# Kernel tuning notes

Measured on AMD Instinct MI355X. Metric: run time of the kernel, lower is better.

The kernel has to match this reference:

```python
import jax, jax.numpy as jnp
import numpy as np

DIM = 1024
HEADS = 16
DIM_HEAD = 64
SEQ = 2048
BATCH = 2
SCALE = DIM_HEAD ** -0.5
NEG = -jnp.finfo(jnp.float32).max


def setup_inputs() -> dict:
    key = jax.random.key(0)
    k1, k2, k3 = jax.random.split(key, 3)
    x = jax.random.normal(k1, (BATCH, SEQ, DIM), dtype=jnp.float32)
    w_qkv = jax.random.normal(k2, (DIM, 3 * HEADS * DIM_HEAD), dtype=jnp.float32) * 0.02
    w_out = jax.random.normal(k3, (HEADS * DIM_HEAD, DIM), dtype=jnp.float32) * 0.02
    b_out = jnp.zeros((DIM,), dtype=jnp.float32)
    return {"x": x, "w_qkv": w_qkv, "w_out": w_out, "b_out": b_out}


def reference(x, w_qkv, w_out, b_out):
    b, n, _ = x.shape
    qkv = x @ w_qkv  # [b, n, 3*h*d]
    q, k, v = jnp.split(qkv, 3, axis=-1)
    def to_heads(t):
        return t.reshape(b, n, HEADS, DIM_HEAD).transpose(0, 2, 1, 3)  # b h n d
    q, k, v = to_heads(q), to_heads(k), to_heads(v)
    q = q * SCALE
    dots = jnp.einsum('bhid,bhjd->bhij', q, k)  # materialized [b,h,n,n] scores
    causal_mask = jnp.triu(jnp.ones((n, n), dtype=bool), k=1)
    dots = jnp.where(causal_mask, NEG, dots)
    attn = jax.nn.softmax(dots, axis=-1)
    out = jnp.einsum('bhij,bhjd->bhid', attn, v)
    out = out.transpose(0, 2, 1, 3).reshape(b, n, HEADS * DIM_HEAD)
    return out @ w_out + b_out
```

## Files before the change

### kernel.cpp

```cpp
#include <hip/hip_runtime.h>
#include <cstdint>

typedef __attribute__((ext_vector_type(8))) short bfrag_t;
typedef __attribute__((ext_vector_type(4))) float f32x4_t;

#define MFMA16(a,b,c) __builtin_amdgcn_mfma_f32_16x16x32_bf16((a),(b),(c),0,0,0)

__device__ __forceinline__ unsigned short f2bf(float f){
  unsigned u = __float_as_uint(f);
  unsigned r = u + 0x7fffu + ((u >> 16) & 1u);
  return (unsigned short)(r >> 16);
}

__device__ __forceinline__ unsigned pk2bf(float a, float b){
  unsigned r;
  asm("v_cvt_pk_bf16_f32 %0, %1, %2" : "=v"(r) : "v"(a), "v"(b));
  return r;
}

__device__ __forceinline__ void gload16(const unsigned short* g, unsigned short* l){
  __builtin_amdgcn_global_load_lds(
      (const __attribute__((address_space(1))) unsigned int*)(const void*)g,
      (__attribute__((address_space(3))) unsigned int*)(void*)l,
      16, 0, 0);
}

__global__ __launch_bounds__(256) void k_cvt(const float* __restrict__ in,
                                             unsigned short* __restrict__ out, int n4){
  int i = blockIdx.x*blockDim.x + threadIdx.x;
  int stride = gridDim.x*blockDim.x;
  for(; i < n4; i += stride){
    float4 v = ((const float4*)in)[i];
    ushort4 o;
    o.x = f2bf(v.x); o.y = f2bf(v.y); o.z = f2bf(v.z); o.w = f2bf(v.w);
    ((ushort4*)out)[i] = o;
  }
}

__global__ __launch_bounds__(256) void k_transpose(const float* __restrict__ in,
                                                   unsigned short* __restrict__ out,
                                                   int R, int C){
  __shared__ unsigned short tile[32][33];
  int bc = blockIdx.x*32, br = blockIdx.y*32;
  int tx = threadIdx.x & 31, ty = threadIdx.x >> 5;
  #pragma unroll
  for(int i=0;i<32;i+=8){
    tile[ty+i][tx] = f2bf(in[(size_t)(br+ty+i)*C + bc + tx]);
  }
  __syncthreads();
  #pragma unroll
  for(int i=0;i<32;i+=8){
    out[(size_t)(bc+ty+i)*R + br + tx] = tile[tx][ty+i];
  }
}

__global__ __launch_bounds__(256) void k_gemm1(
    const unsigned short* __restrict__ A,
    const unsigned short* __restrict__ Bt,
    unsigned short* __restrict__ Qo, unsigned short* __restrict__ Kimg,
    unsigned short* __restrict__ Vimg)
{
  __shared__ unsigned short ldsA[128*64];
  __shared__ unsigned short ldsB[128*64];

  const int tid = threadIdx.x;
  const int lane = tid & 63;
  const int w = tid >> 6;
  const int wr = w >> 1, wc = w & 1;
  const int col16 = lane & 15, g = lane >> 4;
  const int bm = blockIdx.y * 128;
  const int bn = blockIdx.x * 128;
  const int K = 1024;
  const int SWAP = (bn < 2048) ? 1 : 0;

  f32x4_t acc[4][4];
  #pragma unroll
  for(int i=0;i<4;i++)
    #pragma unroll
    for(int j=0;j<4;j++) acc[i][j] = (f32x4_t)0.0f;

  for(int k0=0; k0<K; k0+=64){
    __syncthreads();
    #pragma unroll
    for(int i=0; i<4; i++){
      int u = i*256 + tid;
      int row = u>>3, s = u&7, gs = s ^ (row&7);
      gload16(A + (size_t)(bm+row)*K + k0 + gs*8, ldsA + (i*256 + w*64)*8);
    }
    #pragma unroll
    for(int i=0; i<4; i++){
      int u = i*256 + tid;
      int row = u>>3, s = u&7, gs = s ^ (row&7);
      gload16(Bt + (size_t)(bn+row)*K + k0 + gs*8, ldsB + (i*256 + w*64)*8);
    }
    __syncthreads();
    #pragma unroll
    for(int kk=0; kk<2; kk++){
      bfrag_t af[4], bfr[4];
      #pragma unroll
      for(int mi=0;mi<4;mi++){
        int row = wr*64 + mi*16 + col16;
        int slot = (kk*4 + g) ^ (row&7);
        af[mi] = *(const bfrag_t*)(ldsA + row*64 + slot*8);
      }
      #pragma unroll
      for(int ni=0;ni<4;ni++){
        int row = wc*64 + ni*16 + col16;
        int slot = (kk*4 + g) ^ (row&7);
        bfr[ni] = *(const bfrag_t*)(ldsB + row*64 + slot*8);
      }
      if (SWAP){
        #pragma unroll
        for(int mi=0;mi<4;mi++)
          #pragma unroll
          for(int ni=0;ni<4;ni++)
            acc[mi][ni] = MFMA16(bfr[ni], af[mi], acc[mi][ni]);
      } else {
        #pragma unroll
        for(int mi=0;mi<4;mi++)
          #pragma unroll
          for(int ni=0;ni<4;ni++)
            acc[mi][ni] = MFMA16(af[mi], bfr[ni], acc[mi][ni]);
      }
    }
  }

  if (bn < 2048){
    const int which = bn >> 10;
    #pragma unroll
    for(int mi=0;mi<4;mi++){
      int s_full = bm + wr*64 + mi*16 + col16;
      int b = s_full >> 11, sq = s_full & 2047;
      #pragma unroll
      for(int ni=0;ni<4;ni++){
        int n0 = bn + wc*64 + ni*16 + g*4;
        int h = (n0 & 1023) >> 6;
        int d0 = n0 & 63;
        size_t bh = (size_t)(b*16 + h);
        float v0 = acc[mi][ni][0], v1 = acc[mi][ni][1];
        float v2 = acc[mi][ni][2], v3 = acc[mi][ni][3];
        if (which == 0){
          const float sc = 0.18033688f;
          uint2 pkd; pkd.x = pk2bf(v0*sc, v1*sc); pkd.y = pk2bf(v2*sc, v3*sc);
          *(uint2*)(Qo + (bh*2048 + sq)*64 + d0) = pkd;
        } else {
          int kt = sq >> 6, rr = sq & 63;
          int ks = rr >> 4, c16i = rr & 15;
          int dk = d0 >> 5, g3 = (d0 >> 3) & 3, e0 = d0 & 7;
          uint2 pkd; pkd.x = pk2bf(v0, v1); pkd.y = pk2bf(v2, v3);
          size_t off = bh*131072 + (size_t)kt*4096
                     + (size_t)(ks*2 + dk)*512 + (size_t)(g3*16 + c16i)*8 + e0;
          *(uint2*)(Kimg + off) = pkd;
        }
      }
    }
  } else {
    #pragma unroll
    for(int mi=0;mi<4;mi++){
      int s0 = bm + wr*64 + mi*16 + g*4;
      int b = s0 >> 11, sq0 = s0 & 2047;
      int kt = sq0 >> 6, sc0 = sq0 & 63;
      int jk = sc0 >> 5, g3 = (sc0 >> 3) & 3, e0 = sc0 & 7;
      #pragma unroll
      for(int ni=0;ni<4;ni++){
        int ncol = bn + wc*64 + ni*16 + col16;
        int h = (ncol & 1023) >> 6;
        int d64 = ncol & 63;
        int nimg = d64 >> 4, c16i = d64 & 15;
        size_t bh = (size_t)(b*16 + h);
        uint2 pkd;
        pkd.x = pk2bf(acc[mi][ni][0], acc[mi][ni][1]);
        pkd.y = pk2bf(acc[mi][ni][2], acc[mi][ni][3]);
        size_t off = bh*131072 + (size_t)kt*4096
                   + (size_t)(nimg*2 + jk)*512 + (size_t)(g3*16 + c16i)*8 + e0;
        *(uint2*)(Vimg + off) = pkd;
      }
    }
  }
}

__global__ __launch_bounds__(256) void k_gemm2(
    const unsigned short* __restrict__ A,
    const unsigned short* __restrict__ Bt,
    float* __restrict__ Co, const float* __restrict__ bias)
{
  __shared__ unsigned short ldsA[64*64];
  __shared__ unsigned short ldsB[128*64];

  const int tid = threadIdx.x;
  const int lane = tid & 63;
  const int w = tid >> 6;
  const int wc = w;
  const int col16 = lane & 15, g = lane >> 4;
  const int bm = blockIdx.y * 64;
  const int bn = blockIdx.x * 128;
  const int K = 1024, N = 1024;

  f32x4_t acc[4][2];
  #pragma unroll
  for(int i=0;i<4;i++)
    #pragma unroll
    for(int j=0;j<2;j++) acc[i][j] = (f32x4_t)0.0f;

  for(int k0=0; k0<K; k0+=64){
    __syncthreads();
    #pragma unroll
    for(int i=0; i<2; i++){
      int u = i*256 + tid;
      int row = u>>3, s = u&7, gs = s ^ (row&7);
      gload16(A + (size_t)(bm+row)*K + k0 + gs*8, ldsA + (i*256 + w*64)*8);
    }
    #pragma unroll
    for(int i=0; i<4; i++){
      int u = i*256 + tid;
      int row = u>>3, s = u&7, gs = s ^ (row&7);
      gload16(Bt + (size_t)(bn+row)*K + k0 + gs*8, ldsB + (i*256 + w*64)*8);
    }
    __syncthreads();
    #pragma unroll
    for(int kk=0; kk<2; kk++){
      bfrag_t af[4], bfr[2];
      #pragma unroll
      for(int mi=0;mi<4;mi++){
        int row = mi*16 + col16;
        int slot = (kk*4 + g) ^ (row&7);
        af[mi] = *(const bfrag_t*)(ldsA + row*64 + slot*8);
      }
      #pragma unroll
      for(int ni=0;ni<2;ni++){
        int row = wc*32 + ni*16 + col16;
        int slot = (kk*4 + g) ^ (row&7);
        bfr[ni] = *(const bfrag_t*)(ldsB + row*64 + slot*8);
      }
      #pragma unroll
      for(int mi=0;mi<4;mi++)
        #pragma unroll
        for(int ni=0;ni<2;ni++)
          acc[mi][ni] = MFMA16(af[mi], bfr[ni], acc[mi][ni]);
    }
  }

  #pragma unroll
  for(int mi=0;mi<4;mi++){
    int mrow = bm + mi*16 + g*4;
    #pragma unroll
    for(int ni=0;ni<2;ni++){
      int ncol = bn + wc*32 + ni*16 + col16;
      float bb = bias[ncol];
      #pragma unroll
      for(int r=0;r<4;r++){
        Co[(size_t)(mrow+r)*N + ncol] = acc[mi][ni][r] + bb;
      }
    }
  }
}

__global__ __launch_bounds__(256, 4) void k_attn(
    const unsigned short* __restrict__ Q,
    const unsigned short* __restrict__ Kimg,
    const unsigned short* __restrict__ Vimg,
    unsigned short* __restrict__ O)
{
  __shared__ unsigned short kls[2*4096];
  __shared__ unsigned short vls[2*4096];
  __shared__ unsigned short plds[4*1024];
  const int lane = threadIdx.x & 63;
  const int w = threadIdx.x >> 6;
  const int col16 = lane & 15, g = lane >> 4;
  const int bh = blockIdx.x;
  const int y = blockIdx.y;
  const int idx = (y & 7)*4 + (y >> 3);
  const int qt = (idx & 1) ? (31 - (idx >> 1)) : (idx >> 1);
  const int b = bh >> 4, h = bh & 15;

  const unsigned short* Qb = Q    + (size_t)bh*2048*64;
  const unsigned short* Kb = Kimg + (size_t)bh*131072;
  const unsigned short* Vb = Vimg + (size_t)bh*131072;
  char* pw = (char*)(plds + w*1024);

  auto stage = [&](int kt, int bsel){
    const unsigned short* gk = Kb + (size_t)kt*4096;
    const unsigned short* gv = Vb + (size_t)kt*4096;
    unsigned short* lk = kls + bsel*4096;
    unsigned short* lv = vls + bsel*4096;
    #pragma unroll
    for(int c=0;c<2;c++){
      int chunk = w*2 + c;
      int u = chunk*64 + lane;
      gload16(gk + u*8, lk + chunk*512);
      gload16(gv + u*8, lv + chunk*512);
    }
  };

  const int qrow0 = qt*64 + w*16;
  const int nkt = qt + 1;
  const int qi = qrow0 + col16;

  bfrag_t qf[2];
  #pragma unroll
  for(int dk=0;dk<2;dk++)
    qf[dk] = *(const bfrag_t*)(Qb + (size_t)(qrow0 + col16)*64 + dk*32 + g*8);

  f32x4_t oaccT[4];
  #pragma unroll
  for(int n=0;n<4;n++) oaccT[n] = (f32x4_t)0.0f;
  float mrun = -1e30f, lrun = 0.f;

  stage(0, 0);
  __syncthreads();

  #pragma unroll 1
  for(int kt=0; kt<nkt; kt++){
    const int cur = kt & 1;
    if (kt+1 < nkt) stage(kt+1, cur^1);

    const bfrag_t* kb = (const bfrag_t*)(kls + cur*4096);
    const bfrag_t* vb = (const bfrag_t*)(vls + cur*4096);

    f32x4_t sacc[4];
    __builtin_amdgcn_s_setprio(1);
    #pragma unroll
    for(int ks=0; ks<4; ks++){
      bfrag_t kf0 = kb[(ks*2+0)*64 + lane];
      bfrag_t kf1 = kb[(ks*2+1)*64 + lane];
      f32x4_t c = (f32x4_t)0.0f;
      c = MFMA16(kf0, qf[0], c);
      c = MFMA16(kf1, qf[1], c);
      sacc[ks] = c;
    }
    __builtin_amdgcn_s_setprio(0);
    if (kt == qt){
      const int kbase = kt*64;
      #pragma unroll
      for(int ks=0; ks<4; ks++)
        #pragma unroll
        for(int r=0;r<4;r++){
          int kj = kbase + ks*16 + g*4 + r;
          if (kj > qi) sacc[ks][r] = -1e30f;
        }
    }
    float pm = fmaxf(
        fmaxf(fmaxf(fmaxf(sacc[0][0],sacc[0][1]),fmaxf(sacc[0][2],sacc[0][3])),
              fmaxf(fmaxf(sacc[1][0],sacc[1][1]),fmaxf(sacc[1][2],sacc[1][3]))),
        fmaxf(fmaxf(fmaxf(sacc[2][0],sacc[2][1]),fmaxf(sacc[2][2],sacc[2][3])),
              fmaxf(fmaxf(sacc[3][0],sacc[3][1]),fmaxf(sacc[3][2],sacc[3][3]))));
    pm = fmaxf(pm, __shfl_xor(pm, 16));
    pm = fmaxf(pm, __shfl_xor(pm, 32));
    if (!__all(pm - mrun <= 11.5415603f)){
      float mnew = fmaxf(mrun, pm);
      float alpha = __builtin_amdgcn_exp2f(mrun - mnew);
      mrun = mnew;
      lrun *= alpha;
      #pragma unroll
      for(int n=0;n<4;n++)
        #pragma unroll
        for(int r=0;r<4;r++)
          oaccT[n][r] *= alpha;
    }
    float rs = 0.f;
    #pragma unroll
    for(int ks=0; ks<4; ks++){
      float p0 = __builtin_amdgcn_exp2f(sacc[ks][0] - mrun);
      float p1 = __builtin_amdgcn_exp2f(sacc[ks][1] - mrun);
      float p2 = __builtin_amdgcn_exp2f(sacc[ks][2] - mrun);
      float p3 = __builtin_amdgcn_exp2f(sacc[ks][3] - mrun);
      rs += (p0+p1)+(p2+p3);
      unsigned w0 = pk2bf(p0, p1);
      unsigned w1 = pk2bf(p2, p3);
      int byte0 = (col16*128 + (ks*16 + g*4)*2) ^ ((col16&7)<<4);
      unsigned long long wd = ((unsigned long long)w1 << 32) | w0;
      *(unsigned long long*)(pw + byte0) = wd;
    }
    rs += __shfl_xor(rs, 16);
    rs += __shfl_xor(rs, 32);
    lrun += rs;
    bfrag_t pf[2];
    #pragma unroll
    for(int jk=0;jk<2;jk++){
      int byteo = (col16*128 + jk*64 + g*16) ^ ((col16&7)<<4);
      pf[jk] = *(const bfrag_t*)(pw + byteo);
    }
    __builtin_amdgcn_s_setprio(1);
    #pragma unroll
    for(int n=0;n<4;n++){
      bfrag_t v0 = vb[(n*2+0)*64 + lane];
      bfrag_t v1 = vb[(n*2+1)*64 + lane];
      oaccT[n] = MFMA16(v0, pf[0], oaccT[n]);
      oaccT[n] = MFMA16(v1, pf[1], oaccT[n]);
    }
    __builtin_amdgcn_s_setprio(0);
    __syncthreads();
  }

  {
    float inv = 1.0f / lrun;
    size_t obase = ((size_t)(b*2048 + qi))*1024 + (size_t)h*64;
    #pragma unroll
    for(int n=0;n<4;n++){
      uint2 pkd;
      pkd.x = pk2bf(oaccT[n][0]*inv, oaccT[n][1]*inv);
      pkd.y = pk2bf(oaccT[n][2]*inv, oaccT[n][3]*inv);
      *(uint2*)(O + obase + n*16 + g*4) = pkd;
    }
  }
}

extern "C" void kernel_launch(void* const* d_in, const int* in_sizes, int n_in,
                              void* d_out, int out_size, void* d_ws, size_t ws_size,
                              hipStream_t stream){
  const float* x     = (const float*)d_in[0];
  const float* w_qkv = (const float*)d_in[1];
  const float* w_out = (const float*)d_in[2];
  const float* b_out = (const float*)d_in[3];
  float* out = (float*)d_out;

  unsigned char* ws = (unsigned char*)d_ws;
  unsigned short* xbf   = (unsigned short*)(ws);
  unsigned short* wqkvT = (unsigned short*)(ws + (size_t)8*1024*1024);
  unsigned short* woutT = (unsigned short*)(ws + (size_t)14*1024*1024);
  unsigned short* Qb    = (unsigned short*)(ws + (size_t)16*1024*1024);
  unsigned short* Kb    = (unsigned short*)(ws + (size_t)24*1024*1024);
  unsigned short* Vtb   = (unsigned short*)(ws + (size_t)32*1024*1024);
  unsigned short* attno = xbf;

  k_cvt<<<2048, 256, 0, stream>>>(x, xbf, 4096*1024/4);
  k_transpose<<<dim3(3072/32, 1024/32), 256, 0, stream>>>(w_qkv, wqkvT, 1024, 3072);
  k_transpose<<<dim3(1024/32, 1024/32), 256, 0, stream>>>(w_out, woutT, 1024, 1024);
  k_gemm1<<<dim3(24, 32), 256, 0, stream>>>(xbf, wqkvT, Qb, Kb, Vtb);
  k_attn<<<dim3(32, 32), 256, 0, stream>>>(Qb, Kb, Vtb, attno);
  k_gemm2<<<dim3(8, 64), 256, 0, stream>>>(attno, woutT, out, b_out);
}
```

Before: 117.8 us.

## Fuse input prep kernels and swizzle GEMM block order across XCDs

```diff
diff --git a/kernel.cpp b/kernel.cpp
--- a/kernel.cpp
+++ b/kernel.cpp
@@ -25,24 +25,36 @@
       16, 0, 0);
 }
 
-__global__ __launch_bounds__(256) void k_cvt(const float* __restrict__ in,
-                                             unsigned short* __restrict__ out, int n4){
-  int i = blockIdx.x*blockDim.x + threadIdx.x;
-  int stride = gridDim.x*blockDim.x;
-  for(; i < n4; i += stride){
-    float4 v = ((const float4*)in)[i];
-    ushort4 o;
-    o.x = f2bf(v.x); o.y = f2bf(v.y); o.z = f2bf(v.z); o.w = f2bf(v.w);
-    ((ushort4*)out)[i] = o;
-  }
-}
-
-__global__ __launch_bounds__(256) void k_transpose(const float* __restrict__ in,
-                                                   unsigned short* __restrict__ out,
-                                                   int R, int C){
+__global__ __launch_bounds__(256) void k_prep(
+    const float* __restrict__ x,     unsigned short* __restrict__ xbf,
+    const float* __restrict__ wqkv,  unsigned short* __restrict__ wqkvT,
+    const float* __restrict__ wout,  unsigned short* __restrict__ woutT)
+{
   __shared__ unsigned short tile[32][33];
-  int bc = blockIdx.x*32, br = blockIdx.y*32;
-  int tx = threadIdx.x & 31, ty = threadIdx.x >> 5;
+  const int bid = blockIdx.x;
+  const int tid = threadIdx.x;
+
+  if (bid < 2048){
+    const int n4 = 4096*1024/4;
+    int i = bid*256 + tid;
+    #pragma unroll
+    for(int it=0; it<2; it++, i += 2048*256){
+      if (i < n4){
+        float4 v = ((const float4*)x)[i];
+        ushort4 o;
+        o.x = f2bf(v.x); o.y = f2bf(v.y); o.z = f2bf(v.z); o.w = f2bf(v.w);
+        ((ushort4*)xbf)[i] = o;
+      }
+    }
+    return;
+  }
+
+  const float* in; unsigned short* out; int R, C, idx;
+  if (bid < 5120){ in = wqkv; out = wqkvT; R = 1024; C = 3072; idx = bid - 2048; }
+  else           { in = wout; out = woutT; R = 1024; C = 1024; idx = bid - 5120; }
+  const int nbc = C >> 5;
+  const int bc = (idx % nbc) * 32, br = (idx / nbc) * 32;
+  const int tx = tid & 31, ty = tid >> 5;
   #pragma unroll
   for(int i=0;i<32;i+=8){
     tile[ty+i][tx] = f2bf(in[(size_t)(br+ty+i)*C + bc + tx]);
@@ -68,8 +80,11 @@
   const int w = tid >> 6;
   const int wr = w >> 1, wc = w & 1;
   const int col16 = lane & 15, g = lane >> 4;
-  const int bm = blockIdx.y * 128;
-  const int bn = blockIdx.x * 128;
+
+  const int L = blockIdx.x;
+  const int swz = (L & 7) * 96 + (L >> 3);
+  const int bm = (swz / 24) * 128;
+  const int bn = (swz % 24) * 128;
   const int K = 1024;
   const int SWAP = (bn < 2048) ? 1 : 0;
 
@@ -192,8 +207,11 @@
   const int w = tid >> 6;
   const int wc = w;
   const int col16 = lane & 15, g = lane >> 4;
-  const int bm = blockIdx.y * 64;
-  const int bn = blockIdx.x * 128;
+
+  const int L = blockIdx.x;
+  const int swz = (L & 7) * 64 + (L >> 3);
+  const int bm = (swz >> 3) * 64;
+  const int bn = (swz & 7) * 128;
   const int K = 1024, N = 1024;
 
   f32x4_t acc[4][2];
@@ -423,10 +441,8 @@
   unsigned short* Vtb   = (unsigned short*)(ws + (size_t)32*1024*1024);
   unsigned short* attno = xbf;
 
-  k_cvt<<<2048, 256, 0, stream>>>(x, xbf, 4096*1024/4);
-  k_transpose<<<dim3(3072/32, 1024/32), 256, 0, stream>>>(w_qkv, wqkvT, 1024, 3072);
-  k_transpose<<<dim3(1024/32, 1024/32), 256, 0, stream>>>(w_out, woutT, 1024, 1024);
-  k_gemm1<<<dim3(24, 32), 256, 0, stream>>>(xbf, wqkvT, Qb, Kb, Vtb);
+  k_prep<<<6144, 256, 0, stream>>>(x, xbf, w_qkv, wqkvT, w_out, woutT);
+  k_gemm1<<<768, 256, 0, stream>>>(xbf, wqkvT, Qb, Kb, Vtb);
   k_attn<<<dim3(32, 32), 256, 0, stream>>>(Qb, Kb, Vtb, attno);
-  k_gemm2<<<dim3(8, 64), 256, 0, stream>>>(attno, woutT, out, b_out);
-}
+  k_gemm2<<<512, 256, 0, stream>>>(attno, woutT, out, b_out);
+}
```

After: 111.5 us. -5.4%, faster.
